# Optimization experiments

Hardware: AMD Instinct MI355X
Metric: run time of the kernel (lower is better)

The kernel has to match this reference:

```python
import jax, jax.numpy as jnp
import numpy as np

INPUT_SIZE = 1024
HIDDEN_SIZE = 2048
BATCH = 8192


def setup_inputs() -> dict:
    key = jax.random.key(0)
    k1, k2, k3, k4, k5 = jax.random.split(key, 5)
    input_tensor = jax.random.normal(k1, (BATCH, INPUT_SIZE), dtype=jnp.float32)
    h_0 = jax.random.normal(k2, (BATCH, HIDDEN_SIZE), dtype=jnp.float32)
    c_0 = jax.random.normal(k3, (BATCH, HIDDEN_SIZE), dtype=jnp.float32)
    # parameters: weight [input_size, 3*hidden], weight_hidden [hidden, 3*hidden], bias [3*hidden]
    weight = jax.random.normal(k4, (INPUT_SIZE, 3 * HIDDEN_SIZE), dtype=jnp.float32) * 0.02
    weight_hidden = jax.random.normal(k5, (HIDDEN_SIZE, 3 * HIDDEN_SIZE), dtype=jnp.float32) * 0.02
    bias = jnp.zeros((3 * HIDDEN_SIZE,), dtype=jnp.float32)
    return {
        "input_tensor": input_tensor,
        "h_0": h_0,
        "c_0": c_0,
        "weight": weight,
        "weight_hidden": weight_hidden,
        "bias": bias,
    }


def reference(input_tensor, h_0, c_0, weight, weight_hidden, bias):
    hidden_size = h_0.shape[-1]
    # pre-activations: x @ W + h_0 @ W_h + b  -> [batch, 3*hidden]
    gates = input_tensor @ weight + h_0 @ weight_hidden + bias
    f, i, c = jnp.split(gates, 3, axis=1)
    # c_1 = sigmoid(f) * c_0 + sigmoid(i) * tanh(c)
    c_1 = jax.nn.sigmoid(f) * c_0 + jax.nn.sigmoid(i) * jnp.tanh(c)
    return c_1
```

## Files before the change

kernel.cpp:

```cpp
#include <hip/hip_runtime.h>
#include <stdint.h>


#define BATCH 8192
#define INSZ  1024
#define HID   2048
#define NG    6144
#define KTOT  3072
#define KTILES 96

typedef __attribute__((ext_vector_type(8))) short short8;
typedef __attribute__((ext_vector_type(4))) short short4v;
typedef __attribute__((ext_vector_type(4))) float f32x4;
typedef __attribute__((ext_vector_type(4))) unsigned short u16x4;

__device__ __forceinline__ unsigned short f32_to_bf16(float f) {
  uint32_t u = __builtin_bit_cast(uint32_t, f);
  u += 0x7fffu + ((u >> 16) & 1u);
  return (unsigned short)(u >> 16);
}


__global__ __launch_bounds__(256) void pack_a_kernel(
    const float* __restrict__ x, const float* __restrict__ h,
    unsigned short* __restrict__ Ap) {
  uint32_t q   = blockIdx.x * 256u + threadIdx.x;
  uint32_t kk4 = q & 7u;
  uint32_t m   = (q >> 3) & 8191u;
  uint32_t kt  = q >> 16;
  uint32_t k   = kt * 32u + kk4 * 4u;
  const float* src = (k < INSZ) ? (x + (size_t)m * INSZ + k)
                                : (h + (size_t)m * HID + (k - INSZ));
  float4 v = *(const float4*)src;
  u16x4 o;
  o.x = f32_to_bf16(v.x); o.y = f32_to_bf16(v.y);
  o.z = f32_to_bf16(v.z); o.w = f32_to_bf16(v.w);
  uint32_t c  = kk4 >> 1, hh = kk4 & 1;
  uint32_t sm = (m + (m >> 2)) & 3u;
  *(u16x4*)(Ap + ((size_t)kt * BATCH + m) * 32 + ((c ^ sm) * 8 + hh * 4)) = o;
}

__global__ __launch_bounds__(256) void pack_b_kernel(
    const float* __restrict__ W, const float* __restrict__ Wh,
    unsigned short* __restrict__ Bp) {
  uint32_t q  = blockIdx.x * 256u + threadIdx.x;
  uint32_t hh = q & 7u;
  uint32_t r  = q >> 3;
  uint32_t n  = r % 6144u;
  uint32_t kt = r / 6144u;
  uint32_t k0 = kt * 32u + hh * 4u;
  float v[4];
#pragma unroll
  for (int t = 0; t < 4; ++t) {
    uint32_t k = k0 + t;
    v[t] = (k < INSZ) ? W[(size_t)k * NG + n]
                      : Wh[(size_t)(k - INSZ) * NG + n];
  }
  u16x4 o;
  o.x = f32_to_bf16(v[0]); o.y = f32_to_bf16(v[1]);
  o.z = f32_to_bf16(v[2]); o.w = f32_to_bf16(v[3]);
  *(u16x4*)(Bp + ((size_t)kt * NG + n) * 32 + hh * 4) = o;
}

__device__ __forceinline__ void lstm_epilogue(
    const f32x4 acc[4][6], int m0, int j0, int wm, int wn, int quad, int l16,
    const float* __restrict__ bias, const float* __restrict__ c0,
    float* __restrict__ out) {
#pragma unroll
  for (int mi = 0; mi < 4; ++mi) {
    int rowb = m0 + wm * 64 + mi * 16 + quad * 4;
#pragma unroll
    for (int p = 0; p < 2; ++p) {
      int j = j0 + (2 * wn + p) * 16 + l16;
      float bfv = bias[j], biv = bias[HID + j], bcv = bias[2 * HID + j];
#pragma unroll
      for (int r = 0; r < 4; ++r) {
        size_t idx = (size_t)(rowb + r) * HID + j;
        float fg = acc[mi][0 + p][r] + bfv;
        float ig = acc[mi][2 + p][r] + biv;
        float cg = acc[mi][4 + p][r] + bcv;
        float sf = 1.f / (1.f + __expf(-fg));
        float si = 1.f / (1.f + __expf(-ig));
        float th = 2.f / (1.f + __expf(-2.f * cg)) - 1.f;
        out[idx] = sf * c0[idx] + si * th;
      }
    }
  }
}

__global__ __launch_bounds__(256) void gemm_packed_kernel(
    const unsigned short* __restrict__ Ap, const unsigned short* __restrict__ Bp,
    const float* __restrict__ bias, const float* __restrict__ c0,
    float* __restrict__ out) {
  __shared__ __align__(16) unsigned short As[128 * 32];
  const int tid = threadIdx.x;
  const int lane = tid & 63, w = tid >> 6;
  const int wm = w >> 1, wn = w & 1;
  const int quad = lane >> 4, l16 = lane & 15;
  const int bx = blockIdx.x;
  const int mt = bx & 63, jt = bx >> 6;
  const int m0 = mt * 128, j0 = jt * 64;
  const int sw = (l16 + (l16 >> 2)) & 3;

  f32x4 acc[4][6];
#pragma unroll
  for (int a = 0; a < 4; ++a)
#pragma unroll
    for (int b = 0; b < 6; ++b) acc[a][b] = (f32x4){0.f, 0.f, 0.f, 0.f};

  const unsigned short* bb =
      Bp + ((size_t)(j0 + 2 * wn * 16 + l16)) * 32 + quad * 8;

  short8 bf[2][6];
#pragma unroll
  for (int g = 0; g < 3; ++g)
#pragma unroll
    for (int p = 0; p < 2; ++p)
      bf[0][g * 2 + p] = *(const short8*)(bb + g * (HID * 32) + p * 512);

#pragma unroll 2
  for (int kt = 0; kt < KTILES; ++kt) {
    const int cur = kt & 1;
    const unsigned short* ga = Ap + ((size_t)kt * BATCH + m0) * 32;
#pragma unroll
    for (int i = 0; i < 2; ++i) {
      int t2 = w * 2 + i;
      __builtin_amdgcn_global_load_lds(
          (__attribute__((address_space(1))) void*)(void*)(ga + t2 * 512 + lane * 8),
          (__attribute__((address_space(3))) void*)(As + t2 * 512), 16, 0, 0);
    }
    __syncthreads();
    if (kt + 1 < KTILES) {
      const unsigned short* bn = bb + (size_t)(kt + 1) * (NG * 32);
#pragma unroll
      for (int g = 0; g < 3; ++g)
#pragma unroll
        for (int p = 0; p < 2; ++p)
          bf[cur ^ 1][g * 2 + p] = *(const short8*)(bn + g * (HID * 32) + p * 512);
    }
    short8 af[4];
#pragma unroll
    for (int mi = 0; mi < 4; ++mi)
      af[mi] = *(const short8*)(
          As + (wm * 64 + mi * 16 + l16) * 32 + ((quad ^ sw) * 8));
#pragma unroll
    for (int mi = 0; mi < 4; ++mi)
#pragma unroll
      for (int f = 0; f < 6; ++f)
        acc[mi][f] =
            __builtin_amdgcn_mfma_f32_16x16x32_bf16(af[mi], bf[cur][f], acc[mi][f], 0, 0, 0);
    __syncthreads();
  }
  lstm_epilogue(acc, m0, j0, wm, wn, quad, l16, bias, c0, out);
}

__global__ __launch_bounds__(256) void gemm_f32_kernel(
    const float* __restrict__ x, const float* __restrict__ h,
    const float* __restrict__ W, const float* __restrict__ Wh,
    const float* __restrict__ bias, const float* __restrict__ c0,
    float* __restrict__ out) {
  __shared__ __align__(16) unsigned short As[128 * 36];
  __shared__ __align__(16) unsigned short Bs[192 * 36];
  const int tid = threadIdx.x;
  const int lane = tid & 63, w = tid >> 6;
  const int wm = w >> 1, wn = w & 1;
  const int quad = lane >> 4, l16 = lane & 15;
  const int bx = blockIdx.x;
  const int jt = bx & 31, mt = bx >> 5;
  const int m0 = mt * 128, j0 = jt * 64;

  f32x4 acc[4][6];
#pragma unroll
  for (int a = 0; a < 4; ++a)
#pragma unroll
    for (int b = 0; b < 6; ++b) acc[a][b] = (f32x4){0.f, 0.f, 0.f, 0.f};

  for (int kt = 0; kt < KTILES; ++kt) {
    int k0 = kt * 32;
#pragma unroll
    for (int i = 0; i < 4; ++i) {
      int q = i * 256 + tid;
      int m = q >> 3, kk = (q & 7) * 4;
      int k = k0 + kk;
      const float* src = (k < INSZ) ? (x + (size_t)(m0 + m) * INSZ + k)
                                    : (h + (size_t)(m0 + m) * HID + (k - INSZ));
      float4 v = *(const float4*)src;
      u16x4 o;
      o.x = f32_to_bf16(v.x); o.y = f32_to_bf16(v.y);
      o.z = f32_to_bf16(v.z); o.w = f32_to_bf16(v.w);
      *(u16x4*)(As + m * 36 + kk) = o;
    }
#pragma unroll
    for (int i = 0; i < 6; ++i) {
      int q = i * 256 + tid;
      int n = q % 192, kq = (q / 192) * 4;
      int col = (n >> 6) * HID + j0 + (n & 63);
      float vv[4];
#pragma unroll
      for (int t = 0; t < 4; ++t) {
        int k = k0 + kq + t;
        vv[t] = (k < INSZ) ? W[(size_t)k * NG + col]
                           : Wh[(size_t)(k - INSZ) * NG + col];
      }
      u16x4 o;
      o.x = f32_to_bf16(vv[0]); o.y = f32_to_bf16(vv[1]);
      o.z = f32_to_bf16(vv[2]); o.w = f32_to_bf16(vv[3]);
      *(u16x4*)(Bs + n * 36 + kq) = o;
    }
    __syncthreads();
    short8 af[4], bf[6];
#pragma unroll
    for (int mi = 0; mi < 4; ++mi) {
      int base = (wm * 64 + mi * 16 + l16) * 36 + quad * 8;
      short4v lo = *(const short4v*)(As + base);
      short4v hi = *(const short4v*)(As + base + 4);
      af[mi] = __builtin_shufflevector(lo, hi, 0, 1, 2, 3, 4, 5, 6, 7);
    }
#pragma unroll
    for (int g = 0; g < 3; ++g)
#pragma unroll
      for (int p = 0; p < 2; ++p) {
        int base = (g * 64 + (2 * wn + p) * 16 + l16) * 36 + quad * 8;
        short4v lo = *(const short4v*)(Bs + base);
        short4v hi = *(const short4v*)(Bs + base + 4);
        bf[g * 2 + p] = __builtin_shufflevector(lo, hi, 0, 1, 2, 3, 4, 5, 6, 7);
      }
#pragma unroll
    for (int mi = 0; mi < 4; ++mi)
#pragma unroll
      for (int f = 0; f < 6; ++f)
        acc[mi][f] =
            __builtin_amdgcn_mfma_f32_16x16x32_bf16(af[mi], bf[f], acc[mi][f], 0, 0, 0);
    __syncthreads();
  }
  lstm_epilogue(acc, m0, j0, wm, wn, quad, l16, bias, c0, out);
}

extern "C" void kernel_launch(void* const* d_in, const int* in_sizes, int n_in,
                              void* d_out, int out_size, void* d_ws, size_t ws_size,
                              hipStream_t stream) {
  const float* x    = (const float*)d_in[0];
  const float* h0   = (const float*)d_in[1];
  const float* c0   = (const float*)d_in[2];
  const float* W    = (const float*)d_in[3];
  const float* Wh   = (const float*)d_in[4];
  const float* bias = (const float*)d_in[5];
  float* out = (float*)d_out;

  const size_t needA = (size_t)KTOT * BATCH * 2;
  const size_t needB = (size_t)KTOT * NG * 2;
  if (ws_size >= needA + needB) {
    unsigned short* Ap = (unsigned short*)d_ws;
    unsigned short* Bp = Ap + (size_t)KTOT * BATCH;
    pack_a_kernel<<<24576, 256, 0, stream>>>(x, h0, Ap);
    pack_b_kernel<<<18432, 256, 0, stream>>>(W, Wh, Bp);
    gemm_packed_kernel<<<2048, 256, 0, stream>>>(Ap, Bp, bias, c0, out);
  } else {
    gemm_f32_kernel<<<2048, 256, 0, stream>>>(x, h0, W, Wh, bias, c0, out);
  }
}
```

Measured before the change: 634.4 us.

## Double-buffer A tile in LDS, remap blocks per XCD, raise MFMA priority

Measured after the change: 997.2 us. +57.2%, slower.

```diff
diff --git a/kernel.cpp b/kernel.cpp
--- a/kernel.cpp
+++ b/kernel.cpp
@@ -92,13 +92,15 @@
     const unsigned short* __restrict__ Ap, const unsigned short* __restrict__ Bp,
     const float* __restrict__ bias, const float* __restrict__ c0,
     float* __restrict__ out) {
-  __shared__ __align__(16) unsigned short As[128 * 32];
+  __shared__ __align__(16) unsigned short As[2][128 * 32];
   const int tid = threadIdx.x;
   const int lane = tid & 63, w = tid >> 6;
   const int wm = w >> 1, wn = w & 1;
   const int quad = lane >> 4, l16 = lane & 15;
   const int bx = blockIdx.x;
-  const int mt = bx & 63, jt = bx >> 6;
+  const int xcd = bx & 7, blin = bx >> 3;
+  const int jt = blin & 31;
+  const int mt = ((blin >> 5) << 3) | xcd;
   const int m0 = mt * 128, j0 = jt * 64;
   const int sw = (l16 + (l16 >> 2)) & 3;
 
@@ -111,27 +113,40 @@
   const unsigned short* bb =
       Bp + ((size_t)(j0 + 2 * wn * 16 + l16)) * 32 + quad * 8;
 
-  short8 bf[2][6];
-#pragma unroll
-  for (int g = 0; g < 3; ++g)
-#pragma unroll
-    for (int p = 0; p < 2; ++p)
-      bf[0][g * 2 + p] = *(const short8*)(bb + g * (HID * 32) + p * 512);
-
-#pragma unroll 2
-  for (int kt = 0; kt < KTILES; ++kt) {
-    const int cur = kt & 1;
-    const unsigned short* ga = Ap + ((size_t)kt * BATCH + m0) * 32;
+  {
+    const unsigned short* ga = Ap + (size_t)m0 * 32;
 #pragma unroll
     for (int i = 0; i < 2; ++i) {
       int t2 = w * 2 + i;
       __builtin_amdgcn_global_load_lds(
           (__attribute__((address_space(1))) void*)(void*)(ga + t2 * 512 + lane * 8),
-          (__attribute__((address_space(3))) void*)(As + t2 * 512), 16, 0, 0);
-    }
-    __syncthreads();
+          (__attribute__((address_space(3))) void*)(&As[0][0] + t2 * 512), 16, 0, 0);
+    }
+  }
+  short8 bf[2][6];
+#pragma unroll
+  for (int g = 0; g < 3; ++g)
+#pragma unroll
+    for (int p = 0; p < 2; ++p)
+      bf[0][g * 2 + p] = *(const short8*)(bb + g * (HID * 32) + p * 512);
+  asm volatile("s_waitcnt vmcnt(0)" ::: "memory");
+  __builtin_amdgcn_s_barrier();
+  __builtin_amdgcn_sched_barrier(0);
+
+#pragma unroll 2
+  for (int kt = 0; kt < KTILES; ++kt) {
+    const int cur = kt & 1;
     if (kt + 1 < KTILES) {
-      const unsigned short* bn = bb + (size_t)(kt + 1) * (NG * 32);
+      const unsigned short* ga = Ap + ((size_t)(kt + 1) * BATCH + m0) * 32;
+#pragma unroll
+      for (int i = 0; i < 2; ++i) {
+        int t2 = w * 2 + i;
+        __builtin_amdgcn_global_load_lds(
+            (__attribute__((address_space(1))) void*)(void*)(ga + t2 * 512 + lane * 8),
+            (__attribute__((address_space(3))) void*)(&As[cur ^ 1][0] + t2 * 512),
+            16, 0, 0);
+      }
+      const unsigned short* bn = bb + (size_t)(kt + 1) * ((size_t)NG * 32);
 #pragma unroll
       for (int g = 0; g < 3; ++g)
 #pragma unroll
@@ -142,14 +157,18 @@
 #pragma unroll
     for (int mi = 0; mi < 4; ++mi)
       af[mi] = *(const short8*)(
-          As + (wm * 64 + mi * 16 + l16) * 32 + ((quad ^ sw) * 8));
+          &As[cur][0] + (wm * 64 + mi * 16 + l16) * 32 + ((quad ^ sw) * 8));
+    __builtin_amdgcn_s_setprio(1);
 #pragma unroll
     for (int mi = 0; mi < 4; ++mi)
 #pragma unroll
       for (int f = 0; f < 6; ++f)
         acc[mi][f] =
             __builtin_amdgcn_mfma_f32_16x16x32_bf16(af[mi], bf[cur][f], acc[mi][f], 0, 0, 0);
-    __syncthreads();
+    __builtin_amdgcn_s_setprio(0);
+    asm volatile("s_waitcnt vmcnt(0) lgkmcnt(0)" ::: "memory");
+    __builtin_amdgcn_s_barrier();
+    __builtin_amdgcn_sched_barrier(0);
   }
   lstm_epilogue(acc, m0, j0, wm, wn, quad, l16, bias, c0, out);
 }
```

## Triple-buffer A tiles with explicit waitcnt pipelining and merge pack kernels

Applied to the files above, without the earlier changes.

Measured after the change: 824.6 us. 1.3x slower.

```diff
diff --git a/kernel.cpp b/kernel.cpp
--- a/kernel.cpp
+++ b/kernel.cpp
@@ -20,46 +20,46 @@
   return (unsigned short)(u >> 16);
 }
 
-
-__global__ __launch_bounds__(256) void pack_a_kernel(
+#define PACKA_BLOCKS 24576
+#define PACKB_BLOCKS 18432
+__global__ __launch_bounds__(256) void pack_ab_kernel(
     const float* __restrict__ x, const float* __restrict__ h,
-    unsigned short* __restrict__ Ap) {
-  uint32_t q   = blockIdx.x * 256u + threadIdx.x;
-  uint32_t kk4 = q & 7u;
-  uint32_t m   = (q >> 3) & 8191u;
-  uint32_t kt  = q >> 16;
-  uint32_t k   = kt * 32u + kk4 * 4u;
-  const float* src = (k < INSZ) ? (x + (size_t)m * INSZ + k)
-                                : (h + (size_t)m * HID + (k - INSZ));
-  float4 v = *(const float4*)src;
-  u16x4 o;
-  o.x = f32_to_bf16(v.x); o.y = f32_to_bf16(v.y);
-  o.z = f32_to_bf16(v.z); o.w = f32_to_bf16(v.w);
-  uint32_t c  = kk4 >> 1, hh = kk4 & 1;
-  uint32_t sm = (m + (m >> 2)) & 3u;
-  *(u16x4*)(Ap + ((size_t)kt * BATCH + m) * 32 + ((c ^ sm) * 8 + hh * 4)) = o;
-}
-
-__global__ __launch_bounds__(256) void pack_b_kernel(
     const float* __restrict__ W, const float* __restrict__ Wh,
-    unsigned short* __restrict__ Bp) {
-  uint32_t q  = blockIdx.x * 256u + threadIdx.x;
-  uint32_t hh = q & 7u;
-  uint32_t r  = q >> 3;
-  uint32_t n  = r % 6144u;
-  uint32_t kt = r / 6144u;
-  uint32_t k0 = kt * 32u + hh * 4u;
-  float v[4];
-#pragma unroll
-  for (int t = 0; t < 4; ++t) {
-    uint32_t k = k0 + t;
-    v[t] = (k < INSZ) ? W[(size_t)k * NG + n]
-                      : Wh[(size_t)(k - INSZ) * NG + n];
-  }
-  u16x4 o;
-  o.x = f32_to_bf16(v[0]); o.y = f32_to_bf16(v[1]);
-  o.z = f32_to_bf16(v[2]); o.w = f32_to_bf16(v[3]);
-  *(u16x4*)(Bp + ((size_t)kt * NG + n) * 32 + hh * 4) = o;
+    unsigned short* __restrict__ Ap, unsigned short* __restrict__ Bp) {
+  if (blockIdx.x < PACKA_BLOCKS) {
+    uint32_t q   = blockIdx.x * 256u + threadIdx.x;
+    uint32_t kk4 = q & 7u;
+    uint32_t m   = (q >> 3) & 8191u;
+    uint32_t kt  = q >> 16;
+    uint32_t k   = kt * 32u + kk4 * 4u;
+    const float* src = (k < INSZ) ? (x + (size_t)m * INSZ + k)
+                                  : (h + (size_t)m * HID + (k - INSZ));
+    float4 v = *(const float4*)src;
+    u16x4 o;
+    o.x = f32_to_bf16(v.x); o.y = f32_to_bf16(v.y);
+    o.z = f32_to_bf16(v.z); o.w = f32_to_bf16(v.w);
+    uint32_t c  = kk4 >> 1, hh = kk4 & 1;
+    uint32_t sm = (m + (m >> 2)) & 3u;
+    *(u16x4*)(Ap + ((size_t)kt * BATCH + m) * 32 + ((c ^ sm) * 8 + hh * 4)) = o;
+  } else {
+    uint32_t q  = (blockIdx.x - PACKA_BLOCKS) * 256u + threadIdx.x;
+    uint32_t hh = q & 7u;
+    uint32_t r  = q >> 3;
+    uint32_t n  = r % 6144u;
+    uint32_t kt = r / 6144u;
+    uint32_t k0 = kt * 32u + hh * 4u;
+    float v[4];
+#pragma unroll
+    for (int t = 0; t < 4; ++t) {
+      uint32_t k = k0 + t;
+      v[t] = (k < INSZ) ? W[(size_t)k * NG + n]
+                        : Wh[(size_t)(k - INSZ) * NG + n];
+    }
+    u16x4 o;
+    o.x = f32_to_bf16(v[0]); o.y = f32_to_bf16(v[1]);
+    o.z = f32_to_bf16(v[2]); o.w = f32_to_bf16(v[3]);
+    *(u16x4*)(Bp + ((size_t)kt * NG + n) * 32 + hh * 4) = o;
+  }
 }
 
 __device__ __forceinline__ void lstm_epilogue(
@@ -92,7 +92,7 @@
     const unsigned short* __restrict__ Ap, const unsigned short* __restrict__ Bp,
     const float* __restrict__ bias, const float* __restrict__ c0,
     float* __restrict__ out) {
-  __shared__ __align__(16) unsigned short As[128 * 32];
+  __shared__ __align__(16) unsigned short As[3][128 * 32];
   const int tid = threadIdx.x;
   const int lane = tid & 63, w = tid >> 6;
   const int wm = w >> 1, wn = w & 1;
@@ -111,46 +111,65 @@
   const unsigned short* bb =
       Bp + ((size_t)(j0 + 2 * wn * 16 + l16)) * 32 + quad * 8;
 
+#define STAGE_A(ktile, buf)                                                    \
+  {                                                                            \
+    const unsigned short* ga = Ap + ((size_t)(ktile) * BATCH + m0) * 32;       \
+    _Pragma("unroll")                                                          \
+    for (int i = 0; i < 2; ++i) {                                              \
+      int t2 = w * 2 + i;                                                      \
+      __builtin_amdgcn_global_load_lds(                                        \
+          (__attribute__((address_space(1))) void*)(void*)(ga + t2 * 512 +     \
+                                                           lane * 8),          \
+          (__attribute__((address_space(3))) void*)(&As[(buf)][0] + t2 * 512), \
+          16, 0, 0);                                                           \
+    }                                                                          \
+  }
+
+#define LOAD_B(ktile, idx)                                                     \
+  {                                                                            \
+    const unsigned short* bn = bb + (size_t)(ktile) * ((size_t)NG * 32);       \
+    _Pragma("unroll")                                                          \
+    for (int g = 0; g < 3; ++g)                                                \
+      _Pragma("unroll")                                                        \
+      for (int p = 0; p < 2; ++p)                                              \
+        bf[(idx)][g * 2 + p] = *(const short8*)(bn + g * (HID * 32) + p * 512);\
+  }
+
   short8 bf[2][6];
-#pragma unroll
-  for (int g = 0; g < 3; ++g)
-#pragma unroll
-    for (int p = 0; p < 2; ++p)
-      bf[0][g * 2 + p] = *(const short8*)(bb + g * (HID * 32) + p * 512);
+  STAGE_A(0, 0);
+  STAGE_A(1, 1);
+  LOAD_B(0, 0);
+  asm volatile("s_waitcnt vmcnt(14)" ::: "memory");
+  __builtin_amdgcn_s_barrier();
+  __builtin_amdgcn_sched_barrier(0);
 
 #pragma unroll 2
   for (int kt = 0; kt < KTILES; ++kt) {
     const int cur = kt & 1;
-    const unsigned short* ga = Ap + ((size_t)kt * BATCH + m0) * 32;
-#pragma unroll
-    for (int i = 0; i < 2; ++i) {
-      int t2 = w * 2 + i;
-      __builtin_amdgcn_global_load_lds(
-          (__attribute__((address_space(1))) void*)(void*)(ga + t2 * 512 + lane * 8),
-          (__attribute__((address_space(3))) void*)(As + t2 * 512), 16, 0, 0);
-    }
-    __syncthreads();
-    if (kt + 1 < KTILES) {
-      const unsigned short* bn = bb + (size_t)(kt + 1) * (NG * 32);
-#pragma unroll
-      for (int g = 0; g < 3; ++g)
-#pragma unroll
-        for (int p = 0; p < 2; ++p)
-          bf[cur ^ 1][g * 2 + p] = *(const short8*)(bn + g * (HID * 32) + p * 512);
-    }
+    const int curb = kt % 3;
+    int kt2 = kt + 2; if (kt2 >= KTILES) kt2 = KTILES - 1;
+    int ktb = kt + 1; if (ktb >= KTILES) ktb = KTILES - 1;
+    STAGE_A(kt2, ((kt + 2) % 3));
+    LOAD_B(ktb, cur ^ 1);
     short8 af[4];
 #pragma unroll
     for (int mi = 0; mi < 4; ++mi)
       af[mi] = *(const short8*)(
-          As + (wm * 64 + mi * 16 + l16) * 32 + ((quad ^ sw) * 8));
+          &As[curb][0] + (wm * 64 + mi * 16 + l16) * 32 + ((quad ^ sw) * 8));
+    __builtin_amdgcn_s_setprio(1);
 #pragma unroll
     for (int mi = 0; mi < 4; ++mi)
 #pragma unroll
       for (int f = 0; f < 6; ++f)
         acc[mi][f] =
             __builtin_amdgcn_mfma_f32_16x16x32_bf16(af[mi], bf[cur][f], acc[mi][f], 0, 0, 0);
-    __syncthreads();
-  }
+    __builtin_amdgcn_s_setprio(0);
+    asm volatile("s_waitcnt vmcnt(26)" ::: "memory");
+    __builtin_amdgcn_s_barrier();
+    __builtin_amdgcn_sched_barrier(0);
+  }
+#undef STAGE_A
+#undef LOAD_B
   lstm_epilogue(acc, m0, j0, wm, wn, quad, l16, bias, c0, out);
 }
 
@@ -252,8 +271,7 @@
   if (ws_size >= needA + needB) {
     unsigned short* Ap = (unsigned short*)d_ws;
     unsigned short* Bp = Ap + (size_t)KTOT * BATCH;
-    pack_a_kernel<<<24576, 256, 0, stream>>>(x, h0, Ap);
-    pack_b_kernel<<<18432, 256, 0, stream>>>(W, Wh, Bp);
+    pack_ab_kernel<<<PACKA_BLOCKS + PACKB_BLOCKS, 256, 0, stream>>>(x, h0, W, Wh, Ap, Bp);
     gemm_packed_kernel<<<2048, 256, 0, stream>>>(Ap, Bp, bias, c0, out);
   } else {
     gemm_f32_kernel<<<2048, 256, 0, stream>>>(x, h0, W, Wh, bias, c0, out);
```
